# Kernel tuning notes

Measured on AMD Instinct MI355X. Metric: run time of the kernel, lower is better.

The kernel has to match this reference:

```python
import jax, jax.numpy as jnp
import numpy as np

D = 1024
S = 2048
B = 4


def setup_inputs() -> dict:
    key = jax.random.key(0)
    ks = jax.random.split(key, 9)
    sc = 1.0 / np.sqrt(D)
    return {
        "x": jax.random.normal(ks[0], (B, S, D), dtype=jnp.float32),
        "Wq": jax.random.normal(ks[1], (D, D), dtype=jnp.float32) * sc,
        "bq": jax.random.normal(ks[2], (D,), dtype=jnp.float32) * 0.02,
        "Wk": jax.random.normal(ks[3], (D, D), dtype=jnp.float32) * sc,
        "bk": jax.random.normal(ks[4], (D,), dtype=jnp.float32) * 0.02,
        "Wv": jax.random.normal(ks[5], (D, D), dtype=jnp.float32) * sc,
        "bv": jax.random.normal(ks[6], (D,), dtype=jnp.float32) * 0.02,
        "Wp": jax.random.normal(ks[7], (D, D), dtype=jnp.float32) * sc,
        "bp": jax.random.normal(ks[8], (D,), dtype=jnp.float32) * 0.02,
    }


def reference(x, Wq, bq, Wk, bk, Wv, bv, Wp, bp):
    # torch nn.Linear: y = x @ W.T + b  (W stored [out, in])
    q = jnp.einsum("bsd,ed->bse", x, Wq) + bq  # [B,S,D]
    k = jnp.einsum("bsd,ed->bse", x, Wk) + bk
    v = jnp.einsum("bsd,ed->bse", x, Wv) + bv

    scale = 1.0 / jnp.sqrt(jnp.asarray(q.shape[-1], q.dtype))
    # single-head attention: contract over full embd_dim (no head split in source)
    scores = jnp.einsum("bqd,bkd->bqk", q, k) * scale  # [B,S,S]

    seq = x.shape[1]
    causal = jnp.tril(jnp.ones((seq, seq), dtype=bool))  # [S,S]
    scores = jnp.where(causal[None, :, :], scores, -jnp.inf)

    attn = jax.nn.softmax(scores, axis=-1)  # [B,S,S]
    out = jnp.einsum("bqk,bkd->bqd", attn, v)  # [B,S,D]
    out = jnp.einsum("bsd,ed->bse", out, Wp) + bp
    return out
```

## Files before the change

### kernel.cpp

```cpp
#include <hip/hip_runtime.h>

#define AS1(p) ((const __attribute__((address_space(1))) void*)(p))
#define AS3(p) ((__attribute__((address_space(3))) void*)(p))

typedef unsigned short u16;
typedef __bf16 bf16x8 __attribute__((ext_vector_type(8)));
typedef short s16x8 __attribute__((ext_vector_type(8)));
typedef float f32x4 __attribute__((ext_vector_type(4)));
typedef unsigned short u16x4 __attribute__((ext_vector_type(4)));
typedef unsigned short u16x8v __attribute__((ext_vector_type(8)));

__device__ __forceinline__ u16 f2bf(float x) {
    unsigned u = __float_as_uint(x);
    unsigned r = (u + 0x7FFFu + ((u >> 16) & 1u)) >> 16;
    return (u16)r;
}

template <typename V8>
__device__ __forceinline__ auto mfma_sel(V8 a, V8 b, f32x4 c, int)
    -> decltype(__builtin_amdgcn_mfma_f32_16x16x32_bf16(a, b, c, 0, 0, 0))
{
    return __builtin_amdgcn_mfma_f32_16x16x32_bf16(a, b, c, 0, 0, 0);
}
template <typename V8>
__device__ __forceinline__ f32x4 mfma_sel(V8 a, V8 b, f32x4 c, long)
{
    s16x8 a2 = __builtin_bit_cast(s16x8, a);
    s16x8 b2 = __builtin_bit_cast(s16x8, b);
    return __builtin_amdgcn_mfma_f32_16x16x32_bf16(a2, b2, c, 0, 0, 0);
}
__device__ __forceinline__ f32x4 mfma16x16x32(bf16x8 a, bf16x8 b, f32x4 c)
{
    return mfma_sel(a, b, c, 0);
}

__global__ __launch_bounds__(256) void cvt_all_kernel(const float* __restrict__ x,
                                                      const float* __restrict__ Wq,
                                                      const float* __restrict__ Wk,
                                                      const float* __restrict__ Wv,
                                                      const float* __restrict__ Wp,
                                                      u16* __restrict__ xb,
                                                      u16* __restrict__ Wcat,
                                                      u16* __restrict__ Wpb,
                                                      float* __restrict__ rsum,
                                                      int n4x, int n4w, int nrs)
{
    int i = blockIdx.x * 256 + threadIdx.x;
    const int total = n4x + 4 * n4w;
    if (i >= total) {
        int j = i - total;
        if (j < nrs) rsum[j] = 0.f;
        return;
    }
    const float* src;
    u16* dst;
    int off;
    if (i < n4x) {
        src = x; dst = xb; off = i;
    } else {
        int j = i - n4x;
        int w = j >> 18;
        off = j & (n4w - 1);
        src = (w == 0) ? Wq : (w == 1) ? Wk : (w == 2) ? Wv : Wp;
        dst = (w == 3) ? Wpb : (Wcat + (size_t)w * n4w * 4);
    }
    float4 f = ((const float4*)src)[off];
    u16x4 o;
    o.x = f2bf(f.x); o.y = f2bf(f.y); o.z = f2bf(f.z); o.w = f2bf(f.w);
    ((u16x4*)dst)[off] = o;
}

#define MBM 128
#define MBK 64

template <int BIAS, int OUTBF16, int CSKIP, int CKB, int SWZ, int MW,
          int EXPOUT, int RDIV, int PACKA, int FUSET>
__global__ __launch_bounds__(256, MW)
void gemm128(const u16* __restrict__ A, const u16* __restrict__ B,
             void* __restrict__ Cv, const float* __restrict__ bias,
             void* __restrict__ C2, const float* __restrict__ bias2,
             void* __restrict__ C3, const float* __restrict__ bias3,
             float* __restrict__ rsum,
             int M, int N, int K, int lda, int ldb, int ldc,
             long long sA, long long sB, long long sC, float scale)
{
    __shared__ u16 lA[MBM * MBK];
    __shared__ u16 lB[MBM * MBK];

    if (FUSET && blockIdx.z == 4) {
        const u16* vin = (const u16*)C2;
        u16* vout = (u16*)C3;
        u16* tl = lA;
        const int t = threadIdx.x;
        const int r = t >> 2, c4 = (t & 3) << 4;
        const int bid = blockIdx.y * 16 + blockIdx.x;
        for (int it = 0; it < 8; ++it) {
            const int tile = bid * 8 + it;
            const int tc0 = (tile & 15) * 64;
            const int tr0 = (tile >> 4) * 64;
            const u16* src = vin + (size_t)(tr0 + r) * 1024 + tc0 + c4;
            u16x8v a0 = *(const u16x8v*)src;
            u16x8v a1 = *(const u16x8v*)(src + 8);
            #pragma unroll
            for (int j = 0; j < 8; ++j) {
                tl[r * 65 + c4 + j] = a0[j];
                tl[r * 65 + c4 + 8 + j] = a1[j];
            }
            __syncthreads();
            u16x8v b0, b1;
            #pragma unroll
            for (int j = 0; j < 8; ++j) {
                b0[j] = tl[(c4 + j) * 65 + r];
                b1[j] = tl[(c4 + 8 + j) * 65 + r];
            }
            u16* dst = vout + (size_t)(tc0 + r) * 8192 + tr0 + c4;
            *(u16x8v*)dst = b0;
            *(u16x8v*)(dst + 8) = b1;
            __syncthreads();
        }
        return;
    }

    int bx = blockIdx.x, by = blockIdx.y;
    if (SWZ) {
        const int gx = gridDim.x;
        const int nwg = gx * gridDim.y;
        int id = by * gx + bx;
        id = (id & 7) * (nwg >> 3) + (id >> 3);
        bx = id % gx; by = id / gx;
    }
    if (CKB) by = gridDim.y - 1 - by;
    const int m0 = by * MBM;
    const int n0 = bx * MBM;
    if (CSKIP && n0 > m0 + MBM - 1) return;

    const int z = blockIdx.z;
    const int ablk = m0 >> 7;
    long long abase = (long long)z * sA;
    int lda_e = lda;
    if (PACKA) {
        lda_e = (ablk + 1) << 7;
        abase -= (long long)8192 * ablk * (ablk + 1);
    }
    const u16* Ab = A + abase;
    B += (size_t)z * (size_t)sB;

    const int t = threadIdx.x;
    const int lane = t & 63;
    const int w = t >> 6;
    const int wr = w >> 1;
    const int wc = w & 1;
    const int fr = lane & 15, fg = lane >> 4;

    int Keff = K;
    if (CKB) { Keff = m0 + MBM; if (Keff > K) Keff = K; }
    const int nk = Keff / MBK;

    f32x4 acc[4][4] = {};

    for (int kt = 0; kt < nk; ++kt) {
        const int k0 = kt * MBK;
        #pragma unroll
        for (int i = 0; i < 4; ++i) {
            int c = t + i * 256;
            int row = c >> 3;
            int sl = (c & 7) ^ (row & 7);
            __builtin_amdgcn_global_load_lds(
                AS1(Ab + (long long)(m0 + row) * lda_e + k0 + sl * 8),
                AS3(&lA[c * 8]), 16, 0, 0);
            __builtin_amdgcn_global_load_lds(
                AS1(B + (size_t)(n0 + row) * ldb + k0 + sl * 8),
                AS3(&lB[c * 8]), 16, 0, 0);
        }
        __syncthreads();

        #pragma unroll
        for (int kk = 0; kk < MBK; kk += 32) {
            const int cs = (kk >> 3) + fg;
            bf16x8 af[4], bfv[4];
            #pragma unroll
            for (int mi = 0; mi < 4; ++mi) {
                int row = wr * 64 + mi * 16 + fr;
                af[mi] = *(const bf16x8*)&lA[row * 64 + ((cs ^ (row & 7)) << 3)];
            }
            #pragma unroll
            for (int ni = 0; ni < 4; ++ni) {
                int row = wc * 64 + ni * 16 + fr;
                bfv[ni] = *(const bf16x8*)&lB[row * 64 + ((cs ^ (row & 7)) << 3)];
            }
            __builtin_amdgcn_s_setprio(1);
            #pragma unroll
            for (int mi = 0; mi < 4; ++mi)
                #pragma unroll
                for (int ni = 0; ni < 4; ++ni)
                    acc[mi][ni] = mfma16x16x32(af[mi], bfv[ni], acc[mi][ni]);
            __builtin_amdgcn_s_setprio(0);
        }
        __syncthreads();
    }

    if (EXPOUT) {
        const int ldcp = (ablk + 1) << 7;
        u16* Cp = (u16*)Cv + ((long long)z * sC - (long long)8192 * ablk * (ablk + 1));
        float prs[4][4];
        #pragma unroll
        for (int mi = 0; mi < 4; ++mi)
            #pragma unroll
            for (int j = 0; j < 4; ++j) prs[mi][j] = 0.f;
        #pragma unroll
        for (int mi = 0; mi < 4; ++mi) {
            int row0 = m0 + wr * 64 + mi * 16 + fg * 4;
            #pragma unroll
            for (int ni = 0; ni < 4; ++ni) {
                int col = n0 + wc * 64 + ni * 16 + fr;
                #pragma unroll
                for (int j = 0; j < 4; ++j) {
                    int row = row0 + j;
                    float p = (col <= row) ? __expf(acc[mi][ni][j] - 16.f) : 0.f;
                    Cp[(long long)row * ldcp + col] = f2bf(p);
                    prs[mi][j] += p;
                }
            }
        }
        #pragma unroll
        for (int mi = 0; mi < 4; ++mi) {
            #pragma unroll
            for (int j = 0; j < 4; ++j) {
                float s = prs[mi][j];
                s += __shfl_xor(s, 1); s += __shfl_xor(s, 2);
                s += __shfl_xor(s, 4); s += __shfl_xor(s, 8);
                if (fr == 0)
                    atomicAdd(&rsum[(size_t)z * M + m0 + wr * 64 + mi * 16 + fg * 4 + j], s);
            }
        }
        return;
    }

    #pragma unroll
    for (int mi = 0; mi < 4; ++mi) {
        int row0 = m0 + wr * 64 + mi * 16 + fg * 4;
        float invr[4];
        if (RDIV) {
            #pragma unroll
            for (int j = 0; j < 4; ++j)
                invr[j] = 1.f / rsum[(size_t)z * M + row0 + j];
        }
        #pragma unroll
        for (int ni = 0; ni < 4; ++ni) {
            int col = n0 + wc * 64 + ni * 16 + fr;
            if (BIAS == 3) {
                int seg = col >> 10;
                int ccol = col & 1023;
                u16* dst = (seg == 0) ? (u16*)Cv : (seg == 1) ? (u16*)C2 : (u16*)C3;
                float b = ((seg == 0) ? bias : (seg == 1) ? bias2 : bias3)[ccol];
                float sc_ = (seg == 0) ? scale : 1.f;
                #pragma unroll
                for (int j = 0; j < 4; ++j)
                    dst[(size_t)(row0 + j) * 1024 + ccol] =
                        f2bf((acc[mi][ni][j] + b) * sc_);
            } else {
                float bval = (BIAS == 1) ? bias[col] : 0.f;
                #pragma unroll
                for (int j = 0; j < 4; ++j) {
                    float v = RDIV ? acc[mi][ni][j] * invr[j]
                                   : (acc[mi][ni][j] + bval) * scale;
                    size_t off = (size_t)z * (size_t)sC + (size_t)(row0 + j) * ldc + col;
                    if (OUTBF16) ((u16*)Cv)[off] = f2bf(v);
                    else         ((float*)Cv)[off] = v;
                }
            }
        }
    }
}

extern "C" void kernel_launch(void* const* d_in, const int* in_sizes, int n_in,
                              void* d_out, int out_size, void* d_ws, size_t ws_size,
                              hipStream_t stream)
{
    (void)in_sizes; (void)n_in; (void)out_size; (void)ws_size;
    const float* x  = (const float*)d_in[0];
    const float* Wq = (const float*)d_in[1];
    const float* bq = (const float*)d_in[2];
    const float* Wk = (const float*)d_in[3];
    const float* bk = (const float*)d_in[4];
    const float* Wv = (const float*)d_in[5];
    const float* bv = (const float*)d_in[6];
    const float* Wp = (const float*)d_in[7];
    const float* bp = (const float*)d_in[8];

    const int D = 1024, S = 2048, B = 4;
    const int M = B * S;
    const long long sP = 16384LL * 136;

    char* p = (char*)d_ws;
    u16* xb    = (u16*)p; p += (size_t)M * D * 2;
    u16* Wpb   = (u16*)p; p += (size_t)D * D * 2;
    u16* qb    = (u16*)p; p += (size_t)M * D * 2;
    u16* kb    = (u16*)p; p += (size_t)M * D * 2;
    float* rsum = (float*)p; p += (size_t)B * S * 4;
    u16* vb    = (u16*)p; p += (size_t)M * D * 2;
    u16* scp   = (u16*)p;
    u16* Wcat  = scp;
    u16* vTb   = xb;
    u16* attnb = kb;

    const int n4x = M * D / 4;
    const int n4w = D * D / 4;
    const int nrs = B * S;

    cvt_all_kernel<<<(n4x + 4 * n4w + nrs + 255) / 256, 256, 0, stream>>>(
        x, Wq, Wk, Wv, Wp, xb, Wcat, Wpb, rsum, n4x, n4w, nrs);

    gemm128<3, 1, 0, 0, 1, 3, 0, 0, 0, 0><<<dim3(3 * D / MBM, M / MBM), 256, 0, stream>>>(
        xb, Wcat, qb, bq, kb, bk, vb, bv, nullptr,
        M, 3 * D, D, D, D, D, 0, 0, 0, 0.03125f);

    gemm128<0, 1, 1, 0, 0, 4, 1, 0, 0, 1><<<dim3(S / MBM, S / MBM, B + 1), 256, 0, stream>>>(
        qb, kb, scp, nullptr, vb, nullptr, vTb, nullptr, rsum,
        S, S, D, D, D, 0,
        (long long)S * D, (long long)S * D, sP, 1.0f);

    gemm128<0, 1, 0, 1, 0, 4, 0, 1, 1, 0><<<dim3(D / MBM, S / MBM, B), 256, 0, stream>>>(
        scp, vTb, attnb, nullptr, nullptr, nullptr, nullptr, nullptr, rsum,
        S, D, S, 0, M, D,
        sP, (long long)S, (long long)S * D, 1.0f);

    gemm128<1, 0, 0, 0, 1, 4, 0, 0, 0, 0><<<dim3(D / MBM, M / MBM), 256, 0, stream>>>(
        attnb, Wpb, d_out, bp, nullptr, nullptr, nullptr, nullptr, nullptr,
        M, D, D, D, D, D, 0, 0, 0, 1.0f);
}
```

Before: 180.4 us.

## Add deeper-pipelined GEMM kernel with grouped tile remap for projection GEMMs

```diff
diff --git a/kernel.cpp b/kernel.cpp
--- a/kernel.cpp
+++ b/kernel.cpp
@@ -273,6 +273,142 @@
     }
 }
 
+#define PLDS 81920
+
+template <int BIAS, int OUTBF16>
+__global__ __launch_bounds__(256, 2)
+void gemm128p(const u16* __restrict__ A, const u16* __restrict__ B,
+              void* __restrict__ Cv, const float* __restrict__ bias,
+              void* __restrict__ C2, const float* __restrict__ bias2,
+              void* __restrict__ C3, const float* __restrict__ bias3,
+              int M, int N, int K, int lda, int ldb, int ldc, float scale)
+{
+    extern __shared__ char smem[];
+
+    const int gx = gridDim.x;
+    const int nwg = gx * gridDim.y;
+    int id = blockIdx.y * gx + blockIdx.x;
+    id = (id & 7) * (nwg >> 3) + (id >> 3);
+    const int bx = id % gx;
+    const int by = id / gx;
+    const int m0 = by * MBM;
+    const int n0 = bx * MBM;
+
+    const int t = threadIdx.x;
+    const int lane = t & 63;
+    const int w = t >> 6;
+    const int wr = w >> 1, wc = w & 1;
+    const int fr = lane & 15, fg = lane >> 4;
+
+    const int nk = K / MBK;
+
+    char* const aB = smem;
+    char* const bB = smem + 49152;
+
+    auto STA = [&](int kt, char* dst) {
+        const int k0 = kt * MBK;
+        #pragma unroll
+        for (int i = 0; i < 4; ++i) {
+            int c = t + i * 256;
+            int row = c >> 3;
+            int sl = (c & 7) ^ (row & 7);
+            __builtin_amdgcn_global_load_lds(
+                AS1(A + (size_t)(m0 + row) * lda + k0 + sl * 8),
+                AS3(dst + c * 16), 16, 0, 0);
+        }
+    };
+    auto STB = [&](int kt, char* dst) {
+        const int k0 = kt * MBK;
+        #pragma unroll
+        for (int i = 0; i < 4; ++i) {
+            int c = t + i * 256;
+            int row = c >> 3;
+            int sl = (c & 7) ^ (row & 7);
+            __builtin_amdgcn_global_load_lds(
+                AS1(B + (size_t)(n0 + row) * ldb + k0 + sl * 8),
+                AS3(dst + c * 16), 16, 0, 0);
+        }
+    };
+
+    f32x4 acc[4][4] = {};
+
+    STA(0, aB);
+    STB(0, bB);
+    if (nk > 1) {
+        STA(1, aB + 16384);
+        asm volatile("s_waitcnt vmcnt(4)" ::: "memory");
+    } else {
+        asm volatile("s_waitcnt vmcnt(0)" ::: "memory");
+    }
+    __builtin_amdgcn_s_barrier();
+
+    int ca = 0;
+    for (int kt = 0; kt < nk; ++kt) {
+        if (kt + 1 < nk) STB(kt + 1, bB + ((kt + 1) & 1) * 16384);
+        int pa = ca + 2; if (pa >= 3) pa -= 3;
+        if (kt + 2 < nk) STA(kt + 2, aB + pa * 16384);
+
+        const char* la = aB + ca * 16384;
+        const char* lb = bB + (kt & 1) * 16384;
+        #pragma unroll
+        for (int kk = 0; kk < MBK; kk += 32) {
+            const int cs = (kk >> 3) + fg;
+            bf16x8 af[4], bfv[4];
+            #pragma unroll
+            for (int mi = 0; mi < 4; ++mi) {
+                int row = wr * 64 + mi * 16 + fr;
+                af[mi] = *(const bf16x8*)(la + row * 128 + ((cs ^ (row & 7)) << 4));
+            }
+            #pragma unroll
+            for (int ni = 0; ni < 4; ++ni) {
+                int row = wc * 64 + ni * 16 + fr;
+                bfv[ni] = *(const bf16x8*)(lb + row * 128 + ((cs ^ (row & 7)) << 4));
+            }
+            __builtin_amdgcn_s_setprio(1);
+            #pragma unroll
+            for (int mi = 0; mi < 4; ++mi)
+                #pragma unroll
+                for (int ni = 0; ni < 4; ++ni)
+                    acc[mi][ni] = mfma16x16x32(af[mi], bfv[ni], acc[mi][ni]);
+            __builtin_amdgcn_s_setprio(0);
+        }
+
+        if (kt + 2 < nk)      asm volatile("s_waitcnt vmcnt(4)" ::: "memory");
+        else if (kt + 1 < nk) asm volatile("s_waitcnt vmcnt(0)" ::: "memory");
+        if (kt + 1 < nk) __builtin_amdgcn_s_barrier();
+        ++ca; if (ca >= 3) ca = 0;
+    }
+
+    #pragma unroll
+    for (int mi = 0; mi < 4; ++mi) {
+        int row0 = m0 + wr * 64 + mi * 16 + fg * 4;
+        #pragma unroll
+        for (int ni = 0; ni < 4; ++ni) {
+            int col = n0 + wc * 64 + ni * 16 + fr;
+            if (BIAS == 3) {
+                int seg = col >> 10;
+                int ccol = col & 1023;
+                u16* dst = (seg == 0) ? (u16*)Cv : (seg == 1) ? (u16*)C2 : (u16*)C3;
+                float b = ((seg == 0) ? bias : (seg == 1) ? bias2 : bias3)[ccol];
+                float sc_ = (seg == 0) ? scale : 1.f;
+                #pragma unroll
+                for (int j = 0; j < 4; ++j)
+                    dst[(size_t)(row0 + j) * 1024 + ccol] =
+                        f2bf((acc[mi][ni][j] + b) * sc_);
+            } else {
+                float bval = (BIAS == 1) ? bias[col] : 0.f;
+                #pragma unroll
+                for (int j = 0; j < 4; ++j) {
+                    float v = (acc[mi][ni][j] + bval) * scale;
+                    size_t off = (size_t)(row0 + j) * ldc + col;
+                    if (OUTBF16) ((u16*)Cv)[off] = f2bf(v);
+                    else         ((float*)Cv)[off] = v;
+                }
+            }
+        }
+    }
+}
+
 extern "C" void kernel_launch(void* const* d_in, const int* in_sizes, int n_in,
                               void* d_out, int out_size, void* d_ws, size_t ws_size,
                               hipStream_t stream)
@@ -308,12 +444,17 @@
     const int n4w = D * D / 4;
     const int nrs = B * S;
 
+    hipFuncSetAttribute((const void*)gemm128p<3, 1>,
+                        hipFuncAttributeMaxDynamicSharedMemorySize, PLDS);
+    hipFuncSetAttribute((const void*)gemm128p<1, 0>,
+                        hipFuncAttributeMaxDynamicSharedMemorySize, PLDS);
+
     cvt_all_kernel<<<(n4x + 4 * n4w + nrs + 255) / 256, 256, 0, stream>>>(
         x, Wq, Wk, Wv, Wp, xb, Wcat, Wpb, rsum, n4x, n4w, nrs);
 
-    gemm128<3, 1, 0, 0, 1, 3, 0, 0, 0, 0><<<dim3(3 * D / MBM, M / MBM), 256, 0, stream>>>(
-        xb, Wcat, qb, bq, kb, bk, vb, bv, nullptr,
-        M, 3 * D, D, D, D, D, 0, 0, 0, 0.03125f);
+    gemm128p<3, 1><<<dim3(3 * D / MBM, M / MBM), 256, PLDS, stream>>>(
+        xb, Wcat, qb, bq, kb, bk, vb, bv,
+        M, 3 * D, D, D, D, D, 0.03125f);
 
     gemm128<0, 1, 1, 0, 0, 4, 1, 0, 0, 1><<<dim3(S / MBM, S / MBM, B + 1), 256, 0, stream>>>(
         qb, kb, scp, nullptr, vb, nullptr, vTb, nullptr, rsum,
@@ -325,7 +466,7 @@
         S, D, S, 0, M, D,
         sP, (long long)S, (long long)S * D, 1.0f);
 
-    gemm128<1, 0, 0, 0, 1, 4, 0, 0, 0, 0><<<dim3(D / MBM, M / MBM), 256, 0, stream>>>(
-        attnb, Wpb, d_out, bp, nullptr, nullptr, nullptr, nullptr, nullptr,
-        M, D, D, D, D, D, 0, 0, 0, 1.0f);
-}
+    gemm128p<1, 0><<<dim3(D / MBM, M / MBM), 256, PLDS, stream>>>(
+        attnb, Wpb, d_out, bp, nullptr, nullptr, nullptr, nullptr,
+        M, D, D, D, D, D, 1.0f);
+}
```

New measurement: 175.7 us. 1.03x faster.
